# Optimization experiments

Measured on AMD Instinct MI355X. Metric: run time of the kernel, lower is better.

## Reference

```python
import jax, jax.numpy as jnp
import numpy as np

N_NODES = 50000
N_EDGES = 600000
N_GRAPHS = 512
IN_C, HID_C, OUT_C = 128, 128, 64


def setup_inputs() -> dict:
    key = jax.random.key(0)
    ks = jax.random.split(key, 16)
    inp = {
        "x": jax.random.normal(ks[0], (N_NODES, IN_C), dtype=jnp.float32),
        "edge_index": jax.random.randint(ks[1], (2, N_EDGES), 0, N_NODES, dtype=jnp.int64),
        "batch": jnp.sort(jax.random.randint(ks[2], (N_NODES,), 0, N_GRAPHS, dtype=jnp.int64)),
    }
    # GINConv MLPs: Linear(din,dout) -> ReLU -> Linear(dout,dout)
    dims = [(IN_C, HID_C), (HID_C, HID_C), (HID_C, OUT_C)]
    ki = 3
    for l, (din, dout) in enumerate(dims):
        inp[f"w1_{l}"] = jax.random.normal(ks[ki], (din, dout), jnp.float32) / np.sqrt(din).astype(np.float32)
        inp[f"b1_{l}"] = jnp.zeros((dout,), jnp.float32)
        inp[f"w2_{l}"] = jax.random.normal(ks[ki + 1], (dout, dout), jnp.float32) / np.sqrt(dout).astype(np.float32)
        inp[f"b2_{l}"] = jnp.zeros((dout,), jnp.float32)
        ki += 2
    return inp


def _gin_conv(x, src, dst, w1, b1, w2, b2):
    # sum-aggregate neighbor features: agg[i] = sum_{(j->i) in E} x[j]
    agg = jax.ops.segment_sum(x[src], dst, num_segments=N_NODES)
    h = x + agg  # eps = 0 -> (1+eps)*x + agg
    h = jnp.maximum(h @ w1 + b1, 0.0)
    return h @ w2 + b2


def reference(x, edge_index, batch,
              w1_0, b1_0, w2_0, b2_0,
              w1_1, b1_1, w2_1, b2_1,
              w1_2, b1_2, w2_2, b2_2):
    src, dst = edge_index[0], edge_index[1]
    params = [(w1_0, b1_0, w2_0, b2_0),
              (w1_1, b1_1, w2_1, b2_1),
              (w1_2, b1_2, w2_2, b2_2)]
    # first num_layers-1 convs with outer ReLU
    for l in range(2):
        x = jnp.maximum(_gin_conv(x, src, dst, *params[l]), 0.0)
    x = _gin_conv(x, src, dst, *params[2])
    # global_add_pool over graph ids -> [G, out_channels]
    return jax.ops.segment_sum(x, batch, num_segments=N_GRAPHS)
```

## Files before the change

### kernel.cpp

```cpp
#include <hip/hip_runtime.h>

#define N_NODES 50000
#define N_EDGES 600000
#define N_GRAPHS 512
#define CAP 48

typedef unsigned int u32;
typedef unsigned short u16;
typedef __attribute__((ext_vector_type(8))) short bf16x8;
typedef __attribute__((ext_vector_type(4))) float f32x4;

__device__ __forceinline__ float bflo(u32 v) { return __uint_as_float(v << 16); }
__device__ __forceinline__ float bfhi(u32 v) { return __uint_as_float(v & 0xffff0000u); }
__device__ __forceinline__ u16 f2bf(float f) {
    u32 x = __float_as_uint(f);
    return (u16)((x + 0x7fffu + ((x >> 16) & 1u)) >> 16);
}
__device__ __forceinline__ void addrow(float* a, uint4 v) {
    a[0] += bflo(v.x); a[1] += bfhi(v.x);
    a[2] += bflo(v.y); a[3] += bfhi(v.y);
    a[4] += bflo(v.z); a[5] += bfhi(v.z);
    a[6] += bflo(v.w); a[7] += bfhi(v.w);
}
__device__ __forceinline__ void addrow2(float* a, uint2 v) {
    a[0] += bflo(v.x); a[1] += bfhi(v.x);
    a[2] += bflo(v.y); a[3] += bfhi(v.y);
}

__device__ __forceinline__ int idx_at(const int* __restrict__ a, int i, int wide) {
    return wide ? a[2 * i] : a[i];
}

__global__ void init_kernel(const int* __restrict__ ei, int* __restrict__ cnt,
                            int* __restrict__ flag, float* __restrict__ out,
                            int out_n) {
    int i = blockIdx.x * 256 + threadIdx.x;
    if (i < N_NODES) cnt[i] = 0;
    if (i < out_n) out[i] = 0.f;
    if (blockIdx.x == 0 && threadIdx.x < 64) {
        int v = ei[2 * threadIdx.x + 1];
        unsigned long long nz = __ballot(v != 0);
        if (threadIdx.x == 0) *flag = (nz == 0ull) ? 1 : 0;
    }
}

struct CvtDesc { const float* w; u16* wt; int K, N, bx, bstart; };
struct CvtAll { CvtDesc d[6]; };
struct PrepArgs {
    const int* ei; const int* flag;
    int* cnt; int* slots;
    const float* x; u16* xb;
    CvtAll ca;
};
#define SCAT_B 2344
#define CVTX_B 6250
#define PREP_B (SCAT_B + CVTX_B + 76)

__global__ void prep_kernel(PrepArgs p) {
    int b = blockIdx.x;
    if (b < SCAT_B) {
        int e = b * 256 + threadIdx.x;
        if (e >= N_EDGES) return;
        int w = *p.flag;
        const int* src = p.ei;
        const int* dst = p.ei + (w ? 2 * N_EDGES : N_EDGES);
        int d = idx_at(dst, e, w);
        int pos = atomicAdd(&p.cnt[d], 1);
        if (pos < CAP) p.slots[(size_t)d * CAP + pos] = idx_at(src, e, w);
        return;
    }
    if (b < SCAT_B + CVTX_B) {
        size_t i = (size_t)(b - SCAT_B) * 256 + threadIdx.x;
        float4 v = *(const float4*)&p.x[i * 4];
        u32 o0 = (u32)f2bf(v.x) | ((u32)f2bf(v.y) << 16);
        u32 o1 = (u32)f2bf(v.z) | ((u32)f2bf(v.w) << 16);
        uint2 o; o.x = o0; o.y = o1;
        *(uint2*)&p.xb[i * 4] = o;
        return;
    }
    __shared__ float tile[32][33];
    int rel0 = b - (SCAT_B + CVTX_B);
    int di = 0;
#pragma unroll
    for (int i = 1; i < 6; ++i) if (rel0 >= p.ca.d[i].bstart) di = i;
    CvtDesc d = p.ca.d[di];
    int rel = rel0 - d.bstart;
    int bk = (rel % d.bx) * 32, bn = (rel / d.bx) * 32;
    int tx = threadIdx.x & 31, ty = threadIdx.x >> 5;
#pragma unroll
    for (int yy = 0; yy < 32; yy += 8)
        tile[ty + yy][tx] = d.w[(size_t)(bk + ty + yy) * d.N + bn + tx];
    __syncthreads();
#pragma unroll
    for (int yy = 0; yy < 32; yy += 8)
        d.wt[(size_t)(bn + ty + yy) * d.K + bk + tx] = f2bf(tile[tx][ty + yy]);
}

__global__ void agg128_kernel(const u16* __restrict__ xb, const int* __restrict__ cnt,
                              const int* __restrict__ slots, u16* __restrict__ h) {
    int node = blockIdx.x * 16 + (threadIdx.x >> 4);
    int l = threadIdx.x & 15;
    if (node >= N_NODES) return;
    uint4 sv = *(const uint4*)(xb + ((size_t)node << 7) + l * 8);
    float acc[8] = { bflo(sv.x), bfhi(sv.x), bflo(sv.y), bfhi(sv.y),
                     bflo(sv.z), bfhi(sv.z), bflo(sv.w), bfhi(sv.w) };
    int deg = cnt[node]; if (deg > CAP) deg = CAP;
    const int* sp = slots + (size_t)node * CAP;
    int j = 0;
    for (; j + 4 <= deg; j += 4) {
        int s0 = sp[j], s1 = sp[j + 1], s2 = sp[j + 2], s3 = sp[j + 3];
        uint4 v0 = *(const uint4*)(xb + ((size_t)s0 << 7) + l * 8);
        uint4 v1 = *(const uint4*)(xb + ((size_t)s1 << 7) + l * 8);
        uint4 v2 = *(const uint4*)(xb + ((size_t)s2 << 7) + l * 8);
        uint4 v3 = *(const uint4*)(xb + ((size_t)s3 << 7) + l * 8);
        addrow(acc, v0); addrow(acc, v1);
        addrow(acc, v2); addrow(acc, v3);
    }
    for (; j < deg; ++j) {
        int s0 = sp[j];
        uint4 v0 = *(const uint4*)(xb + ((size_t)s0 << 7) + l * 8);
        addrow(acc, v0);
    }
    uint4 o;
    o.x = (u32)f2bf(acc[0]) | ((u32)f2bf(acc[1]) << 16);
    o.y = (u32)f2bf(acc[2]) | ((u32)f2bf(acc[3]) << 16);
    o.z = (u32)f2bf(acc[4]) | ((u32)f2bf(acc[5]) << 16);
    o.w = (u32)f2bf(acc[6]) | ((u32)f2bf(acc[7]) << 16);
    *(uint4*)(h + ((size_t)node << 7) + l * 8) = o;
}

__global__ void agg64_kernel(const u16* __restrict__ z, const int* __restrict__ cnt,
                             const int* __restrict__ slots,
                             const float* __restrict__ b1, u16* __restrict__ tout) {
    int node = blockIdx.x * 16 + (threadIdx.x >> 4);
    int l = threadIdx.x & 15;
    if (node >= N_NODES) return;
    uint2 sv = *(const uint2*)(z + ((size_t)node << 6) + l * 4);
    float acc[4] = { bflo(sv.x), bfhi(sv.x), bflo(sv.y), bfhi(sv.y) };
    int deg = cnt[node]; if (deg > CAP) deg = CAP;
    const int* sp = slots + (size_t)node * CAP;
    int j = 0;
    for (; j + 4 <= deg; j += 4) {
        int s0 = sp[j], s1 = sp[j + 1], s2 = sp[j + 2], s3 = sp[j + 3];
        uint2 v0 = *(const uint2*)(z + ((size_t)s0 << 6) + l * 4);
        uint2 v1 = *(const uint2*)(z + ((size_t)s1 << 6) + l * 4);
        uint2 v2 = *(const uint2*)(z + ((size_t)s2 << 6) + l * 4);
        uint2 v3 = *(const uint2*)(z + ((size_t)s3 << 6) + l * 4);
        addrow2(acc, v0); addrow2(acc, v1);
        addrow2(acc, v2); addrow2(acc, v3);
    }
    for (; j < deg; ++j) {
        int s0 = sp[j];
        uint2 v0 = *(const uint2*)(z + ((size_t)s0 << 6) + l * 4);
        addrow2(acc, v0);
    }
    float t0 = fmaxf(acc[0] + b1[l * 4 + 0], 0.f);
    float t1 = fmaxf(acc[1] + b1[l * 4 + 1], 0.f);
    float t2 = fmaxf(acc[2] + b1[l * 4 + 2], 0.f);
    float t3 = fmaxf(acc[3] + b1[l * 4 + 3], 0.f);
    uint2 o;
    o.x = (u32)f2bf(t0) | ((u32)f2bf(t1) << 16);
    o.y = (u32)f2bf(t2) | ((u32)f2bf(t3) << 16);
    *(uint2*)(tout + ((size_t)node << 6) + l * 4) = o;
}

template <int CHAIN>
__global__ __launch_bounds__(1024) void mlp_kernel(
    const u16* __restrict__ h,
    const u16* __restrict__ w1t, const float* __restrict__ b1,
    const u16* __restrict__ w2t, const float* __restrict__ b2,
    const u16* __restrict__ w3t, u16* __restrict__ zout,
    u16* __restrict__ yout)
{
    __shared__ __attribute__((aligned(16))) u16 hs[64 * 128];
    __shared__ __attribute__((aligned(16))) u16 ts[64 * 128];
    u16* ybt = hs;

    const int tid = threadIdx.x;
    const int wave = tid >> 6, lane = tid & 63;
    const int base = blockIdx.x * 64;

    {
        int row = tid >> 4, cg = (tid & 15) * 8;
        uint4 v = *(const uint4*)&h[((size_t)(base + row)) * 128 + cg];
        *(uint4*)&hs[row * 128 + (cg ^ ((row & 7) << 3))] = v;
    }
    __syncthreads();

    const int m = lane & 15;
    const int ko = (lane >> 4) * 8;
    const int rb = (wave & 3) * 16;
    const int cbase = (wave >> 2) * 32;

    {
        const int rr = rb + m;
        const int sw = (rr & 7) << 3;
        bf16x8 a1[4];
#pragma unroll
        for (int s = 0; s < 4; ++s)
            a1[s] = *(const bf16x8*)&hs[rr * 128 + ((s * 32 + ko) ^ sw)];
        f32x4 acc[2];
#pragma unroll
        for (int nt = 0; nt < 2; ++nt) acc[nt] = (f32x4){0.f, 0.f, 0.f, 0.f};
#pragma unroll
        for (int nt = 0; nt < 2; ++nt) {
            int n = cbase + nt * 16 + m;
#pragma unroll
            for (int s = 0; s < 4; ++s) {
                bf16x8 bf = *(const bf16x8*)&w1t[(size_t)n * 128 + s * 32 + ko];
                acc[nt] = __builtin_amdgcn_mfma_f32_16x16x32_bf16(a1[s], bf, acc[nt], 0, 0, 0);
            }
        }
#pragma unroll
        for (int nt = 0; nt < 2; ++nt) {
            int n = cbase + nt * 16 + m;
            float bias = b1[n];
#pragma unroll
            for (int j2 = 0; j2 < 4; ++j2) {
                int dr = rb + (lane >> 4) * 4 + j2;
                float v = fmaxf(acc[nt][j2] + bias, 0.f);
                ts[dr * 128 + (n ^ ((dr & 7) << 3))] = f2bf(v);
            }
        }
    }
    __syncthreads();

    {
        const int rr = rb + m;
        const int sw = (rr & 7) << 3;
        bf16x8 a2[4];
#pragma unroll
        for (int s = 0; s < 4; ++s)
            a2[s] = *(const bf16x8*)&ts[rr * 128 + ((s * 32 + ko) ^ sw)];
        f32x4 acc[2];
#pragma unroll
        for (int nt = 0; nt < 2; ++nt) acc[nt] = (f32x4){0.f, 0.f, 0.f, 0.f};
#pragma unroll
        for (int nt = 0; nt < 2; ++nt) {
            int n = cbase + nt * 16 + m;
#pragma unroll
            for (int s = 0; s < 4; ++s) {
                bf16x8 bf = *(const bf16x8*)&w2t[(size_t)n * 128 + s * 32 + ko];
                acc[nt] = __builtin_amdgcn_mfma_f32_16x16x32_bf16(a2[s], bf, acc[nt], 0, 0, 0);
            }
        }
        if (CHAIN) {
#pragma unroll
            for (int nt = 0; nt < 2; ++nt) {
                int n = cbase + nt * 16 + m;
                float bias = b2[n];
#pragma unroll
                for (int j2 = 0; j2 < 4; ++j2) {
                    int dr = rb + (lane >> 4) * 4 + j2;
                    float v = fmaxf(acc[nt][j2] + bias, 0.f);
                    ybt[dr * 128 + (n ^ ((dr & 7) << 3))] = f2bf(v);
                }
            }
        } else {
#pragma unroll
            for (int nt = 0; nt < 2; ++nt) {
                int n = cbase + nt * 16 + m;
                float bias = b2[n];
#pragma unroll
                for (int j2 = 0; j2 < 4; ++j2) {
                    int dr = rb + (lane >> 4) * 4 + j2;
                    int node = base + dr;
                    if (node < N_NODES) {
                        float v = fmaxf(acc[nt][j2] + bias, 0.f);
                        yout[(size_t)node * 128 + n] = f2bf(v);
                    }
                }
            }
        }
    }
    if (CHAIN) {
        __syncthreads();
        const int rr = rb + m;
        const int sw = (rr & 7) << 3;
        const int cb3 = (wave >> 2) * 16;
        bf16x8 a3[4];
#pragma unroll
        for (int s = 0; s < 4; ++s)
            a3[s] = *(const bf16x8*)&ybt[rr * 128 + ((s * 32 + ko) ^ sw)];
        f32x4 acc3 = (f32x4){0.f, 0.f, 0.f, 0.f};
        int n3 = cb3 + m;
#pragma unroll
        for (int s = 0; s < 4; ++s) {
            bf16x8 bf = *(const bf16x8*)&w3t[(size_t)n3 * 128 + s * 32 + ko];
            acc3 = __builtin_amdgcn_mfma_f32_16x16x32_bf16(a3[s], bf, acc3, 0, 0, 0);
        }
#pragma unroll
        for (int j2 = 0; j2 < 4; ++j2) {
            int dr = rb + (lane >> 4) * 4 + j2;
            int node = base + dr;
            if (node < N_NODES)
                zout[(size_t)node * 64 + n3] = f2bf(acc3[j2]);
        }
    }
}

__global__ __launch_bounds__(1024) void pool_kernel(
    const u16* __restrict__ t, const u16* __restrict__ w2t,
    const float* __restrict__ b2,
    const int* __restrict__ batch, const int* __restrict__ flagp,
    float* __restrict__ out)
{
    constexpr int YB_ST = 66;
    __shared__ __attribute__((aligned(16))) char smemA[64 * YB_ST * 4];
    __shared__ int gids[64];
    u16* hs = (u16*)smemA;
    float* yb = (float*)smemA;

    const int tid = threadIdx.x;
    const int wave = tid >> 6, lane = tid & 63;
    const int base = blockIdx.x * 64;
    const int wflag = *flagp;

    if (tid < 64) {
        int node = base + tid;
        gids[tid] = (node < N_NODES) ? idx_at(batch, node, wflag) : -1;
    }
    {
        int row = tid >> 4, c0 = (tid & 15) * 4;
        uint2 v = *(const uint2*)&t[((size_t)(base + row)) * 64 + c0];
        *(uint2*)&hs[row * 64 + (c0 ^ ((row & 7) << 3))] = v;
    }
    __syncthreads();

    const int m = lane & 15;
    const int ko = (lane >> 4) * 8;
    const int rb = (wave & 3) * 16;
    const int cb = (wave >> 2) * 16;

    {
        const int rr = rb + m;
        const int sw = (rr & 7) << 3;
        bf16x8 a2[2];
#pragma unroll
        for (int s = 0; s < 2; ++s)
            a2[s] = *(const bf16x8*)&hs[rr * 64 + ((s * 32 + ko) ^ sw)];
        f32x4 acc = (f32x4){0.f, 0.f, 0.f, 0.f};
        int n = cb + m;
#pragma unroll
        for (int s = 0; s < 2; ++s) {
            bf16x8 bf = *(const bf16x8*)&w2t[(size_t)n * 64 + s * 32 + ko];
            acc = __builtin_amdgcn_mfma_f32_16x16x32_bf16(a2[s], bf, acc, 0, 0, 0);
        }
        float bias = b2[n];
        __syncthreads();
#pragma unroll
        for (int j2 = 0; j2 < 4; ++j2) {
            int dr = rb + (lane >> 4) * 4 + j2;
            yb[dr * YB_ST + n] = acc[j2] + bias;
        }
    }
    __syncthreads();

    {
        int gl = gids[lane];
        int gp = (lane > 0) ? gids[lane - 1] : gl;
        unsigned long long mask = __ballot(lane > 0 && gl != gp) | 1ull;
        int nruns = (int)__popcll(mask);
        int c = tid >> 4, s = tid & 15;
        unsigned long long mm = mask;
        for (int r = 0; r < nruns; ++r) {
            int start = (int)__builtin_ctzll(mm);
            mm &= mm - 1;
            int end = mm ? (int)__builtin_ctzll(mm) : 64;
            int gid = gids[start];
            if (gid >= 0) {
                float sum = 0.f;
                for (int n2 = start + s; n2 < end; n2 += 16)
                    sum += yb[n2 * YB_ST + c];
                sum += __shfl_xor(sum, 1);
                sum += __shfl_xor(sum, 2);
                sum += __shfl_xor(sum, 4);
                sum += __shfl_xor(sum, 8);
                if (s == 0)
                    atomicAdd(&out[(size_t)gid * 64 + c], sum);
            }
        }
    }
}

extern "C" void kernel_launch(void* const* d_in, const int* in_sizes, int n_in,
                              void* d_out, int out_size, void* d_ws, size_t ws_size,
                              hipStream_t stream) {
    const float* x     = (const float*)d_in[0];
    const int*   ei    = (const int*)d_in[1];
    const int*   batch = (const int*)d_in[2];
    const float* w1[3] = {(const float*)d_in[3], (const float*)d_in[7],  (const float*)d_in[11]};
    const float* b1[3] = {(const float*)d_in[4], (const float*)d_in[8],  (const float*)d_in[12]};
    const float* w2[3] = {(const float*)d_in[5], (const float*)d_in[9],  (const float*)d_in[13]};
    const float* b2[3] = {(const float*)d_in[6], (const float*)d_in[10], (const float*)d_in[14]};
    float* out = (float*)d_out;

    char* ws = (char*)d_ws;
    int*   cnt     = (int*)(ws + 0);
    int*   flag    = (int*)(ws + 200704);
    int*   slots   = (int*)(ws + 201728);
    u16*   xb      = (u16*)(ws + 9801728);
    u16*   hbuf    = (u16*)(ws + 22601728);
    u16*   yA      = (u16*)(ws + 35401728);
    u16*   wts     = (u16*)(ws + 48201728);
    u16*   zbuf    = xb;
    u16*   tbuf    = hbuf;
    u16* w1t0 = wts +      0;
    u16* w2t0 = wts +  16384;
    u16* w1t1 = wts +  32768;
    u16* w2t1 = wts +  49152;
    u16* w1t2 = wts +  65536;
    u16* w2t2 = wts +  73728;

    init_kernel<<<196, 256, 0, stream>>>(ei, cnt, flag, out, out_size);

    PrepArgs pa;
    pa.ei = ei; pa.flag = flag; pa.cnt = cnt; pa.slots = slots;
    pa.x = x; pa.xb = xb;
    pa.ca.d[0] = {w1[0], w1t0, 128, 128, 4,  0};
    pa.ca.d[1] = {w2[0], w2t0, 128, 128, 4, 16};
    pa.ca.d[2] = {w1[1], w1t1, 128, 128, 4, 32};
    pa.ca.d[3] = {w2[1], w2t1, 128, 128, 4, 48};
    pa.ca.d[4] = {w1[2], w1t2, 128,  64, 4, 64};
    pa.ca.d[5] = {w2[2], w2t2,  64,  64, 2, 72};
    prep_kernel<<<PREP_B, 256, 0, stream>>>(pa);

    const int NAGG = (N_NODES + 15) / 16;
    const int NTIL = (N_NODES + 63) / 64;

    agg128_kernel<<<NAGG, 256, 0, stream>>>(xb, cnt, slots, hbuf);
    mlp_kernel<0><<<NTIL, 1024, 0, stream>>>(hbuf, w1t0, b1[0], w2t0, b2[0],
                                             (const u16*)0, (u16*)0, yA);
    agg128_kernel<<<NAGG, 256, 0, stream>>>(yA, cnt, slots, hbuf);
    mlp_kernel<1><<<NTIL, 1024, 0, stream>>>(hbuf, w1t1, b1[1], w2t1, b2[1],
                                             w1t2, zbuf, (u16*)0);
    agg64_kernel<<<NAGG, 256, 0, stream>>>(zbuf, cnt, slots, b1[2], tbuf);
    pool_kernel<<<NTIL, 1024, 0, stream>>>(tbuf, w2t2, b2[2], batch, flag, out);
}
```

Before: 198.7 us.

## Write aggregation output in MFMA fragment order and make MLP wave-independent

The aggregation kernel now stores its output in a tiled layout that matches the MFMA A-operand fragment order. Each wave of the MLP kernel can then load its 16-row tile directly from global memory without staging through LDS. The MLP kernel becomes 256-thread blocks in which each wave handles a full 16-row tile through all layers, using per-wave LDS scratch and no block barriers. This trades more weight loads per wave and more accumulator registers for removing __syncthreads and the shared staging of inputs. The pool buffer alias also moves from hbuf to yA.

```diff
diff --git a/kernel.cpp b/kernel.cpp
--- a/kernel.cpp
+++ b/kernel.cpp
@@ -4,6 +4,7 @@
 #define N_EDGES 600000
 #define N_GRAPHS 512
 #define CAP 48
+#define NRT 3125
 
 typedef unsigned int u32;
 typedef unsigned short u16;
@@ -97,7 +98,7 @@
 }
 
 __global__ void agg128_kernel(const u16* __restrict__ xb, const int* __restrict__ cnt,
-                              const int* __restrict__ slots, u16* __restrict__ h) {
+                              const int* __restrict__ slots, u16* __restrict__ h2) {
     int node = blockIdx.x * 16 + (threadIdx.x >> 4);
     int l = threadIdx.x & 15;
     if (node >= N_NODES) return;
@@ -126,7 +127,7 @@
     o.y = (u32)f2bf(acc[2]) | ((u32)f2bf(acc[3]) << 16);
     o.z = (u32)f2bf(acc[4]) | ((u32)f2bf(acc[5]) << 16);
     o.w = (u32)f2bf(acc[6]) | ((u32)f2bf(acc[7]) << 16);
-    *(uint4*)(h + ((size_t)node << 7) + l * 8) = o;
+    *(uint4*)(h2 + (size_t)(node >> 4) * 2048 + l * 128 + (node & 15) * 8) = o;
 }
 
 __global__ void agg64_kernel(const u16* __restrict__ z, const int* __restrict__ cnt,
@@ -165,46 +166,35 @@
 }
 
 template <int CHAIN>
-__global__ __launch_bounds__(1024) void mlp_kernel(
-    const u16* __restrict__ h,
+__global__ __launch_bounds__(256) void mlp_kernel(
+    const u16* __restrict__ h2,
     const u16* __restrict__ w1t, const float* __restrict__ b1,
     const u16* __restrict__ w2t, const float* __restrict__ b2,
     const u16* __restrict__ w3t, u16* __restrict__ zout,
     u16* __restrict__ yout)
 {
-    __shared__ __attribute__((aligned(16))) u16 hs[64 * 128];
-    __shared__ __attribute__((aligned(16))) u16 ts[64 * 128];
-    u16* ybt = hs;
-
-    const int tid = threadIdx.x;
-    const int wave = tid >> 6, lane = tid & 63;
-    const int base = blockIdx.x * 64;
+    __shared__ __attribute__((aligned(16))) u16 ts[4 * 2048];
+    __shared__ __attribute__((aligned(16))) u16 ys[4 * 2048];
+    const int wave = threadIdx.x >> 6, lane = threadIdx.x & 63;
+    const int rtile = blockIdx.x * 4 + wave;
+    if (rtile >= NRT) return;
+    const int m = lane & 15, q = lane >> 4, ko = q * 8;
+    u16* tsw = ts + wave * 2048;
+    u16* ysw = ys + wave * 2048;
+    const u16* hp = h2 + (size_t)rtile * 2048;
+
+    bf16x8 a1[4];
+#pragma unroll
+    for (int s = 0; s < 4; ++s)
+        a1[s] = *(const bf16x8*)&hp[s * 512 + q * 128 + m * 8];
 
     {
-        int row = tid >> 4, cg = (tid & 15) * 8;
-        uint4 v = *(const uint4*)&h[((size_t)(base + row)) * 128 + cg];
-        *(uint4*)&hs[row * 128 + (cg ^ ((row & 7) << 3))] = v;
-    }
-    __syncthreads();
-
-    const int m = lane & 15;
-    const int ko = (lane >> 4) * 8;
-    const int rb = (wave & 3) * 16;
-    const int cbase = (wave >> 2) * 32;
-
-    {
-        const int rr = rb + m;
-        const int sw = (rr & 7) << 3;
-        bf16x8 a1[4];
-#pragma unroll
-        for (int s = 0; s < 4; ++s)
-            a1[s] = *(const bf16x8*)&hs[rr * 128 + ((s * 32 + ko) ^ sw)];
-        f32x4 acc[2];
-#pragma unroll
-        for (int nt = 0; nt < 2; ++nt) acc[nt] = (f32x4){0.f, 0.f, 0.f, 0.f};
-#pragma unroll
-        for (int nt = 0; nt < 2; ++nt) {
-            int n = cbase + nt * 16 + m;
+        f32x4 acc[8];
+#pragma unroll
+        for (int nt = 0; nt < 8; ++nt) acc[nt] = (f32x4){0.f, 0.f, 0.f, 0.f};
+#pragma unroll
+        for (int nt = 0; nt < 8; ++nt) {
+            int n = nt * 16 + m;
 #pragma unroll
             for (int s = 0; s < 4; ++s) {
                 bf16x8 bf = *(const bf16x8*)&w1t[(size_t)n * 128 + s * 32 + ko];
@@ -212,89 +202,85 @@
             }
         }
 #pragma unroll
-        for (int nt = 0; nt < 2; ++nt) {
-            int n = cbase + nt * 16 + m;
+        for (int nt = 0; nt < 8; ++nt) {
+            int n = nt * 16 + m;
             float bias = b1[n];
 #pragma unroll
             for (int j2 = 0; j2 < 4; ++j2) {
-                int dr = rb + (lane >> 4) * 4 + j2;
+                int dr = q * 4 + j2;
                 float v = fmaxf(acc[nt][j2] + bias, 0.f);
-                ts[dr * 128 + (n ^ ((dr & 7) << 3))] = f2bf(v);
-            }
-        }
-    }
-    __syncthreads();
+                tsw[dr * 128 + (n ^ ((dr & 7) << 3))] = f2bf(v);
+            }
+        }
+    }
 
     {
-        const int rr = rb + m;
-        const int sw = (rr & 7) << 3;
+        const int sw = (m & 7) << 3;
         bf16x8 a2[4];
 #pragma unroll
         for (int s = 0; s < 4; ++s)
-            a2[s] = *(const bf16x8*)&ts[rr * 128 + ((s * 32 + ko) ^ sw)];
-        f32x4 acc[2];
-#pragma unroll
-        for (int nt = 0; nt < 2; ++nt) acc[nt] = (f32x4){0.f, 0.f, 0.f, 0.f};
-#pragma unroll
-        for (int nt = 0; nt < 2; ++nt) {
-            int n = cbase + nt * 16 + m;
+            a2[s] = *(const bf16x8*)&tsw[m * 128 + ((s * 32 + ko) ^ sw)];
+        f32x4 acc[8];
+#pragma unroll
+        for (int nt = 0; nt < 8; ++nt) acc[nt] = (f32x4){0.f, 0.f, 0.f, 0.f};
+#pragma unroll
+        for (int nt = 0; nt < 8; ++nt) {
+            int n = nt * 16 + m;
 #pragma unroll
             for (int s = 0; s < 4; ++s) {
                 bf16x8 bf = *(const bf16x8*)&w2t[(size_t)n * 128 + s * 32 + ko];
                 acc[nt] = __builtin_amdgcn_mfma_f32_16x16x32_bf16(a2[s], bf, acc[nt], 0, 0, 0);
             }
         }
-        if (CHAIN) {
-#pragma unroll
-            for (int nt = 0; nt < 2; ++nt) {
-                int n = cbase + nt * 16 + m;
-                float bias = b2[n];
-#pragma unroll
-                for (int j2 = 0; j2 < 4; ++j2) {
-                    int dr = rb + (lane >> 4) * 4 + j2;
-                    float v = fmaxf(acc[nt][j2] + bias, 0.f);
-                    ybt[dr * 128 + (n ^ ((dr & 7) << 3))] = f2bf(v);
-                }
-            }
-        } else {
-#pragma unroll
-            for (int nt = 0; nt < 2; ++nt) {
-                int n = cbase + nt * 16 + m;
-                float bias = b2[n];
-#pragma unroll
-                for (int j2 = 0; j2 < 4; ++j2) {
-                    int dr = rb + (lane >> 4) * 4 + j2;
-                    int node = base + dr;
-                    if (node < N_NODES) {
-                        float v = fmaxf(acc[nt][j2] + bias, 0.f);
-                        yout[(size_t)node * 128 + n] = f2bf(v);
-                    }
-                }
-            }
-        }
-    }
+#pragma unroll
+        for (int nt = 0; nt < 8; ++nt) {
+            int n = nt * 16 + m;
+            float bias = b2[n];
+#pragma unroll
+            for (int j2 = 0; j2 < 4; ++j2) {
+                int dr = q * 4 + j2;
+                float v = fmaxf(acc[nt][j2] + bias, 0.f);
+                ysw[dr * 128 + (n ^ ((dr & 7) << 3))] = f2bf(v);
+            }
+        }
+    }
+
     if (CHAIN) {
-        __syncthreads();
-        const int rr = rb + m;
-        const int sw = (rr & 7) << 3;
-        const int cb3 = (wave >> 2) * 16;
+        const int sw = (m & 7) << 3;
         bf16x8 a3[4];
 #pragma unroll
         for (int s = 0; s < 4; ++s)
-            a3[s] = *(const bf16x8*)&ybt[rr * 128 + ((s * 32 + ko) ^ sw)];
-        f32x4 acc3 = (f32x4){0.f, 0.f, 0.f, 0.f};
-        int n3 = cb3 + m;
-#pragma unroll
-        for (int s = 0; s < 4; ++s) {
-            bf16x8 bf = *(const bf16x8*)&w3t[(size_t)n3 * 128 + s * 32 + ko];
-            acc3 = __builtin_amdgcn_mfma_f32_16x16x32_bf16(a3[s], bf, acc3, 0, 0, 0);
-        }
-#pragma unroll
-        for (int j2 = 0; j2 < 4; ++j2) {
-            int dr = rb + (lane >> 4) * 4 + j2;
-            int node = base + dr;
-            if (node < N_NODES)
-                zout[(size_t)node * 64 + n3] = f2bf(acc3[j2]);
+            a3[s] = *(const bf16x8*)&ysw[m * 128 + ((s * 32 + ko) ^ sw)];
+        f32x4 acc3[4];
+#pragma unroll
+        for (int nt = 0; nt < 4; ++nt) acc3[nt] = (f32x4){0.f, 0.f, 0.f, 0.f};
+#pragma unroll
+        for (int nt = 0; nt < 4; ++nt) {
+            int n3 = nt * 16 + m;
+#pragma unroll
+            for (int s = 0; s < 4; ++s) {
+                bf16x8 bf = *(const bf16x8*)&w3t[(size_t)n3 * 128 + s * 32 + ko];
+                acc3[nt] = __builtin_amdgcn_mfma_f32_16x16x32_bf16(a3[s], bf, acc3[nt], 0, 0, 0);
+            }
+        }
+#pragma unroll
+        for (int nt = 0; nt < 4; ++nt) {
+            int n3 = nt * 16 + m;
+#pragma unroll
+            for (int j2 = 0; j2 < 4; ++j2) {
+                int row = q * 4 + j2;
+                zout[(size_t)(rtile * 16 + row) * 64 + n3] = f2bf(acc3[nt][j2]);
+            }
+        }
+    } else {
+        int r = lane >> 2;
+        int c0 = (lane & 3) * 32;
+        const int sw = (r & 7) << 3;
+#pragma unroll
+        for (int j = 0; j < 4; ++j) {
+            int ce = c0 + j * 8;
+            uint4 v = *(const uint4*)&ysw[r * 128 + (ce ^ sw)];
+            *(uint4*)&yout[(size_t)(rtile * 16 + r) * 128 + ce] = v;
         }
     }
 }
@@ -404,7 +390,7 @@
     u16*   yA      = (u16*)(ws + 35401728);
     u16*   wts     = (u16*)(ws + 48201728);
     u16*   zbuf    = xb;
-    u16*   tbuf    = hbuf;
+    u16*   tbuf    = yA;
     u16* w1t0 = wts +      0;
     u16* w2t0 = wts +  16384;
     u16* w1t1 = wts +  32768;
@@ -429,11 +415,11 @@
     const int NTIL = (N_NODES + 63) / 64;
 
     agg128_kernel<<<NAGG, 256, 0, stream>>>(xb, cnt, slots, hbuf);
-    mlp_kernel<0><<<NTIL, 1024, 0, stream>>>(hbuf, w1t0, b1[0], w2t0, b2[0],
-                                             (const u16*)0, (u16*)0, yA);
+    mlp_kernel<0><<<NTIL, 256, 0, stream>>>(hbuf, w1t0, b1[0], w2t0, b2[0],
+                                            (const u16*)0, (u16*)0, yA);
     agg128_kernel<<<NAGG, 256, 0, stream>>>(yA, cnt, slots, hbuf);
-    mlp_kernel<1><<<NTIL, 1024, 0, stream>>>(hbuf, w1t1, b1[1], w2t1, b2[1],
-                                             w1t2, zbuf, (u16*)0);
+    mlp_kernel<1><<<NTIL, 256, 0, stream>>>(hbuf, w1t1, b1[1], w2t1, b2[1],
+                                            w1t2, zbuf, (u16*)0);
     agg64_kernel<<<NAGG, 256, 0, stream>>>(zbuf, cnt, slots, b1[2], tbuf);
     pool_kernel<<<NTIL, 1024, 0, stream>>>(tbuf, w2t2, b2[2], batch, flag, out);
 }
```

Result: no change. 194.9 us (-1.9%).
